# Kernel tuning notes

Measured on AMD Instinct MI355X. Metric: run time of the kernel, lower is better.

Reference implementation:

```python
import jax, jax.numpy as jnp
import numpy as np

N_NODES = 200_000
N_EDGES = 6_400_000


def _gat_head(h, src, dst, W, a, n_nodes):
    """One GAT head: z = h @ W; e = leaky_relu([z_src||z_dst] @ a);
    segment softmax of e over incoming edges of each dst node;
    weighted scatter-add of z_src into dst. W: [Din, Dout], a: [2*Dout]."""
    d = W.shape[1]
    z = h @ W                      # [N, Dout]
    z_src = z[src]                 # [E, Dout] gather
    z_dst = z[dst]                 # [E, Dout] gather
    # [z_src||z_dst] @ a == z_src @ a[:d] + z_dst @ a[d:]  (avoids materializing the cat)
    e = jax.nn.leaky_relu(z_src @ a[:d] + z_dst @ a[d:])  # [E]
    # numerically stable segment softmax grouped by dst
    m = jax.ops.segment_max(e, dst, num_segments=n_nodes)
    m = jnp.where(jnp.isfinite(m), m, 0.0)
    ex = jnp.exp(e - m[dst])
    denom = jax.ops.segment_sum(ex, dst, num_segments=n_nodes)
    alpha = ex / denom[dst]        # [E]
    # weighted scatter-aggregation; isolated dst nodes get zeros (DGL update_all)
    return jax.ops.segment_sum(alpha[:, None] * z_src, dst, num_segments=n_nodes)


def reference(h, src, dst, fc1, attn1, fc2, attn2, mlp_w, mlp_b):
    n = h.shape[0]
    # layer1: 2 heads, hidden_dim=16, merge='cat' -> [N, 32]
    heads = [_gat_head(h, src, dst, fc1[i], attn1[i], n) for i in range(fc1.shape[0])]
    x = jnp.concatenate(heads, axis=1)
    x = jax.nn.elu(x)
    # layer2: 1 head, out_dim=2, cat of single head -> [N, 2]
    x = _gat_head(x, src, dst, fc2, attn2, n)
    # flatten to [1, 2*N], linear, sigmoid
    x = x.reshape(1, -1)
    out = jax.nn.sigmoid(x @ mlp_w + mlp_b)
    return out


def setup_inputs() -> dict:
    key = jax.random.key(0)
    ks = jax.random.split(key, 9)
    h = jax.random.normal(ks[0], (N_NODES, 2), dtype=jnp.float32)
    src = jax.random.randint(ks[1], (N_EDGES,), 0, N_NODES)
    dst = jax.random.randint(ks[2], (N_EDGES,), 0, N_NODES)
    # layer1: 2 heads, fc [in=2 -> out=16] stored as [head, in, out]; attn [head, 2*16]
    fc1 = jax.random.normal(ks[3], (2, 2, 16), dtype=jnp.float32)
    attn1 = jax.random.normal(ks[4], (2, 32), dtype=jnp.float32)
    # layer2: 1 head, fc [32 -> 2]; attn [2*2]
    fc2 = jax.random.normal(ks[5], (32, 2), dtype=jnp.float32)
    attn2 = jax.random.normal(ks[6], (4,), dtype=jnp.float32)
    # final MLP: Linear(2*num_nodes, 1); small scale to keep sigmoid unsaturated
    mlp_w = jax.random.normal(ks[7], (2 * N_NODES, 1), dtype=jnp.float32) * 1e-3
    mlp_b = jax.random.normal(ks[8], (1,), dtype=jnp.float32)
    return {"h": h, "src": src, "dst": dst, "fc1": fc1, "attn1": attn1,
            "fc2": fc2, "attn2": attn2, "mlp_w": mlp_w, "mlp_b": mlp_b}
```

## Files before the change

### kernel.cpp

```cpp
#include <hip/hip_runtime.h>
#include <hip/hip_bf16.h>
#include <math.h>

#define NN 200000
#define NE 6400000

#define BSHIFT 9
#define BNODES 512
#define NB 391
#define CAP 17408
#define NBLK_SC 256
#define SCT 1024
#define CHUNK (NE / NBLK_SC)

#define W_DACC 0
#define W_UV   4
#define W_CUR  16
#define W_NOFF 2048
#define W_NCNT (W_NOFF + NN)
#define W_META (W_NCNT + NN)
#define W_ACC  (W_META + NB*CAP)
#define W_Z2   (W_ACC + 6*NN)
#define W_TOTAL (W_Z2 + 2*NN)

__global__ void k_init(unsigned* __restrict__ ws) {
    int t = blockIdx.x * blockDim.x + threadIdx.x;
    if (t == 0) *(double*)ws = 0.0;
    if (t < NB) ws[W_CUR + t] = 0u;
}

__global__ void k_prep(const float* __restrict__ fc1, const float* __restrict__ attn1,
                       float* __restrict__ uv) {
    int t = threadIdx.x;
    if (t < 8) {
        int h = t >> 2, r = t & 3, i = r & 1, isv = r >> 1;
        double s = 0.0;
        for (int o = 0; o < 16; ++o)
            s += (double)fc1[h * 32 + i * 16 + o] * (double)attn1[h * 32 + isv * 16 + o];
        uv[t] = (float)s;
    }
}

__launch_bounds__(SCT)
__global__ void k_scatter(const int* __restrict__ src, const int* __restrict__ dst,
                          unsigned* __restrict__ meta, unsigned* __restrict__ cur) {
    __shared__ unsigned cnt[NB], gbase[NB];
    for (int i = threadIdx.x; i < NB; i += SCT) cnt[i] = 0u;
    __syncthreads();
    int beg = blockIdx.x * CHUNK;
    unsigned pack[25];
#pragma unroll
    for (int k = 0; k < 25; ++k) {
        int j = k * SCT + threadIdx.x;
        pack[k] = 0xFFFFFFFFu;
        if (j < CHUNK) {
            unsigned d = (unsigned)__builtin_nontemporal_load(dst + beg + j);
            unsigned rank = atomicAdd(&cnt[d >> BSHIFT], 1u);
            pack[k] = d | (rank << 18);
        }
    }
    __syncthreads();
    for (int i = threadIdx.x; i < NB; i += SCT)
        gbase[i] = cnt[i] ? atomicAdd(&cur[i], cnt[i]) : 0u;
    __syncthreads();
#pragma unroll
    for (int k = 0; k < 25; ++k) {
        if (pack[k] != 0xFFFFFFFFu) {
            int j = k * SCT + threadIdx.x;
            unsigned d = pack[k] & 0x3FFFFu;
            unsigned b = d >> BSHIFT;
            unsigned slot = gbase[b] + (pack[k] >> 18);
            if (slot < CAP) {
                unsigned sn = (unsigned)__builtin_nontemporal_load(src + beg + j);
                meta[(size_t)b * CAP + slot] = sn | ((d & (BNODES - 1)) << 18);
            }
        }
    }
}

__launch_bounds__(1024)
__global__ void k_sort(unsigned* __restrict__ meta, const unsigned* __restrict__ cur,
                       unsigned* __restrict__ nodeoff, unsigned* __restrict__ nodecnt) {
    __shared__ unsigned hist[BNODES], base[BNODES], scan[BNODES];
    int b = blockIdx.x, t = threadIdx.x;
    size_t boff = (size_t)b * CAP;
    int cnt = min((int)cur[b], CAP);
    for (int i = t; i < BNODES; i += 1024) hist[i] = 0u;
    __syncthreads();
    unsigned rm[17], rr[17];
#pragma unroll
    for (int k = 0; k < 17; ++k) {
        int i = k * 1024 + t;
        rm[k] = 0xFFFFFFFFu;
        rr[k] = 0u;
        if (i < cnt) {
            rm[k] = meta[boff + i];
            rr[k] = atomicAdd(&hist[rm[k] >> 18], 1u);
        }
    }
    asm volatile("s_waitcnt vmcnt(0)" ::: "memory");
    __syncthreads();
    if (t < BNODES) scan[t] = hist[t];
    __syncthreads();
    for (int d = 1; d < BNODES; d <<= 1) {
        unsigned v = 0u;
        if (t < BNODES && t >= d) v = scan[t - d];
        __syncthreads();
        if (t < BNODES) scan[t] += v;
        __syncthreads();
    }
    int nb = b * BNODES;
    int nn = min(BNODES, NN - nb);
    if (t < BNODES) {
        unsigned ex = scan[t] - hist[t];
        base[t] = ex;
        if (t < nn) {
            nodeoff[nb + t] = (unsigned)boff + ex;
            nodecnt[nb + t] = hist[t];
        }
    }
    __syncthreads();
#pragma unroll
    for (int k = 0; k < 17; ++k)
        if (rm[k] != 0xFFFFFFFFu)
            meta[boff + base[rm[k] >> 18] + rr[k]] = rm[k];
}

__global__ void k_gat1(const unsigned* __restrict__ meta, const unsigned* __restrict__ nodeoff,
                       const unsigned* __restrict__ nodecnt, const float2* __restrict__ h,
                       const float* __restrict__ uv, float* __restrict__ accc) {
    int n = blockIdx.x * blockDim.x + threadIdx.x;
    if (n >= NN) return;
    float u00 = uv[0], u10 = uv[1], v00 = uv[2], v10 = uv[3];
    float u01 = uv[4], u11 = uv[5], v01 = uv[6], v11 = uv[7];
    float2 hd = h[n];
    float c0 = fmaf(hd.x, v00, hd.y * v10);
    float c1 = fmaf(hd.x, v01, hd.y * v11);
    unsigned off = nodeoff[n];
    int cnt = (int)nodecnt[n];
    float s0 = 0.f, s1 = 0.f, s2 = 0.f, s3 = 0.f, s4 = 0.f, s5 = 0.f;
#pragma unroll 4
    for (int k = 0; k < cnt; ++k) {
        unsigned m = meta[(size_t)off + k];
        float2 hs = h[m & 0x3FFFF];
        float e0 = fmaf(hs.x, u00, fmaf(hs.y, u10, c0));
        float e1 = fmaf(hs.x, u01, fmaf(hs.y, u11, c1));
        e0 = e0 >= 0.f ? e0 : 0.01f * e0;
        e1 = e1 >= 0.f ? e1 : 0.01f * e1;
        float ex0 = __expf(e0);
        float ex1 = __expf(e1);
        s0 += ex0; s1 += ex0 * hs.x; s2 += ex0 * hs.y;
        s3 += ex1; s4 += ex1 * hs.x; s5 += ex1 * hs.y;
    }
    accc[(size_t)0 * NN + n] = s0;
    accc[(size_t)1 * NN + n] = s1;
    accc[(size_t)2 * NN + n] = s2;
    accc[(size_t)3 * NN + n] = s3;
    accc[(size_t)4 * NN + n] = s4;
    accc[(size_t)5 * NN + n] = s5;
}

__global__ void k_node1(const float* __restrict__ accc, const float* __restrict__ fc1,
                        const float* __restrict__ fc2, float2* __restrict__ z2) {
    int n = blockIdx.x * blockDim.x + threadIdx.x;
    if (n >= NN) return;
    float a[6];
#pragma unroll
    for (int j = 0; j < 6; ++j) a[j] = accc[(size_t)j * NN + n];
    float den0 = a[0], A0 = a[1], B0 = a[2];
    float den1 = a[3], A1 = a[4], B1 = a[5];
    float x[32];
#pragma unroll
    for (int o = 0; o < 16; ++o) {
        float t0 = den0 > 0.f ? (A0 * fc1[o]      + B0 * fc1[16 + o]) / den0 : 0.f;
        float t1 = den1 > 0.f ? (A1 * fc1[32 + o] + B1 * fc1[48 + o]) / den1 : 0.f;
        x[o]      = t0 > 0.f ? t0 : expm1f(t0);
        x[16 + o] = t1 > 0.f ? t1 : expm1f(t1);
    }
    float z0 = 0.f, z1 = 0.f;
#pragma unroll
    for (int j = 0; j < 32; ++j) {
        z0 += x[j] * fc2[2 * j];
        z1 += x[j] * fc2[2 * j + 1];
    }
    z2[n] = make_float2(z0, z1);
}

__global__ void k_gat2(const unsigned* __restrict__ meta, const unsigned* __restrict__ nodeoff,
                       const unsigned* __restrict__ nodecnt, const float2* __restrict__ z2,
                       const float* __restrict__ attn2, float* __restrict__ acc2c) {
    int n = blockIdx.x * blockDim.x + threadIdx.x;
    if (n >= NN) return;
    float a0 = attn2[0], a1 = attn2[1], a2 = attn2[2], a3 = attn2[3];
    float2 zd = z2[n];
    float cd = fmaf(zd.x, a2, zd.y * a3);
    unsigned off = nodeoff[n];
    int cnt = (int)nodecnt[n];
    float s0 = 0.f, s1 = 0.f, s2 = 0.f;
#pragma unroll 4
    for (int k = 0; k < cnt; ++k) {
        unsigned m = meta[(size_t)off + k];
        float2 zs = z2[m & 0x3FFFF];
        float e = fmaf(zs.x, a0, fmaf(zs.y, a1, cd));
        e = e >= 0.f ? e : 0.01f * e;
        float ex = __expf(e - 48.f);
        s0 += ex; s1 += ex * zs.x; s2 += ex * zs.y;
    }
    acc2c[(size_t)0 * NN + n] = s0;
    acc2c[(size_t)1 * NN + n] = s1;
    acc2c[(size_t)2 * NN + n] = s2;
}

__global__ void k_final(const float* __restrict__ acc2c, const float* __restrict__ mlp_w,
                        double* __restrict__ dacc) {
    int n = blockIdx.x * blockDim.x + threadIdx.x;
    double v = 0.0;
    if (n < NN) {
        float den = acc2c[(size_t)0 * NN + n];
        float n0  = acc2c[(size_t)1 * NN + n];
        float n1  = acc2c[(size_t)2 * NN + n];
        float x0 = den > 0.f ? n0 / den : 0.f;
        float x1 = den > 0.f ? n1 / den : 0.f;
        v = (double)x0 * (double)mlp_w[2 * n] + (double)x1 * (double)mlp_w[2 * n + 1];
    }
    for (int off = 32; off > 0; off >>= 1) v += __shfl_down(v, off);
    __shared__ double sm[4];
    int lane = threadIdx.x & 63, wid = threadIdx.x >> 6;
    if (lane == 0) sm[wid] = v;
    __syncthreads();
    if (threadIdx.x == 0) {
        double sum = sm[0] + sm[1] + sm[2] + sm[3];
        unsafeAtomicAdd(dacc, sum);
    }
}

__global__ void k_out(const double* __restrict__ dacc, const float* __restrict__ mlp_b,
                      float* __restrict__ out) {
    double logit = dacc[0] + (double)mlp_b[0];
    out[0] = (float)(1.0 / (1.0 + exp(-logit)));
}

extern "C" void kernel_launch(void* const* d_in, const int* in_sizes, int n_in,
                              void* d_out, int out_size, void* d_ws, size_t ws_size,
                              hipStream_t stream) {
    const float* h     = (const float*)d_in[0];
    const int*   src   = (const int*)d_in[1];
    const int*   dst   = (const int*)d_in[2];
    const float* fc1   = (const float*)d_in[3];
    const float* attn1 = (const float*)d_in[4];
    const float* fc2   = (const float*)d_in[5];
    const float* attn2 = (const float*)d_in[6];
    const float* mlp_w = (const float*)d_in[7];
    const float* mlp_b = (const float*)d_in[8];
    float* out = (float*)d_out;

    unsigned* ws      = (unsigned*)d_ws;
    double*   dacc    = (double*)d_ws;
    float*    uv      = (float*)(ws + W_UV);
    unsigned* cur     = ws + W_CUR;
    unsigned* nodeoff = ws + W_NOFF;
    unsigned* nodecnt = ws + W_NCNT;
    unsigned* meta    = ws + W_META;
    float*    accc    = (float*)(ws + W_ACC);
    float2*   z2      = (float2*)(ws + W_Z2);

    const int NG = (NN + 255) / 256;

    hipLaunchKernelGGL(k_init, dim3(2), dim3(256), 0, stream, ws);
    hipLaunchKernelGGL(k_prep, dim3(1), dim3(64), 0, stream, fc1, attn1, uv);
    hipLaunchKernelGGL(k_scatter, dim3(NBLK_SC), dim3(SCT), 0, stream,
                       src, dst, meta, cur);
    hipLaunchKernelGGL(k_sort, dim3(NB), dim3(1024), 0, stream,
                       meta, cur, nodeoff, nodecnt);
    hipLaunchKernelGGL(k_gat1, dim3(NG), dim3(256), 0, stream,
                       meta, nodeoff, nodecnt, (const float2*)h, uv, accc);
    hipLaunchKernelGGL(k_node1, dim3(NG), dim3(256), 0, stream, accc, fc1, fc2, z2);
    hipLaunchKernelGGL(k_gat2, dim3(NG), dim3(256), 0, stream,
                       meta, nodeoff, nodecnt, (const float2*)z2, attn2, accc);
    hipLaunchKernelGGL(k_final, dim3(NG), dim3(256), 0, stream, accc, mlp_w, dacc);
    hipLaunchKernelGGL(k_out, dim3(1), dim3(1), 0, stream, dacc, mlp_b, out);
}
```

Before: 250.6 us.

## Fuse node update into GAT passes and resize destination buckets to match CUs

The per-node layer-1 epilogue (normalise, ELU, project through fc2) moves into k_gat1. The layer-2 normalise and MLP reduction moves into k_gat2. This drops two launches and the intermediate accumulator arrays written to and reread from global memory. The destination bucketing changes from 391 buckets of 512 nodes to 256 buckets of 782 nodes, so k_sort runs one block per CU with more registers per thread. Non-power-of-two buckets need an integer divide in the scatter, and larger per-block sorts raise register pressure.

```diff
diff --git a/kernel.cpp b/kernel.cpp
--- a/kernel.cpp
+++ b/kernel.cpp
@@ -5,22 +5,21 @@
 #define NN 200000
 #define NE 6400000
 
-#define BSHIFT 9
-#define BNODES 512
-#define NB 391
-#define CAP 17408
+#define BNODES 782
+#define NB 256
+#define CAP 27648
 #define NBLK_SC 256
 #define SCT 1024
 #define CHUNK (NE / NBLK_SC)
+#define SREG 27
 
 #define W_DACC 0
 #define W_UV   4
 #define W_CUR  16
-#define W_NOFF 2048
+#define W_NOFF 1024
 #define W_NCNT (W_NOFF + NN)
 #define W_META (W_NCNT + NN)
-#define W_ACC  (W_META + NB*CAP)
-#define W_Z2   (W_ACC + 6*NN)
+#define W_Z2   (W_META + NB*CAP)
 #define W_TOTAL (W_Z2 + 2*NN)
 
 __global__ void k_init(unsigned* __restrict__ ws) {
@@ -55,7 +54,7 @@
         pack[k] = 0xFFFFFFFFu;
         if (j < CHUNK) {
             unsigned d = (unsigned)__builtin_nontemporal_load(dst + beg + j);
-            unsigned rank = atomicAdd(&cnt[d >> BSHIFT], 1u);
+            unsigned rank = atomicAdd(&cnt[d / BNODES], 1u);
             pack[k] = d | (rank << 18);
         }
     }
@@ -68,29 +67,30 @@
         if (pack[k] != 0xFFFFFFFFu) {
             int j = k * SCT + threadIdx.x;
             unsigned d = pack[k] & 0x3FFFFu;
-            unsigned b = d >> BSHIFT;
+            unsigned b = d / BNODES;
+            unsigned dl = d - b * BNODES;
             unsigned slot = gbase[b] + (pack[k] >> 18);
             if (slot < CAP) {
                 unsigned sn = (unsigned)__builtin_nontemporal_load(src + beg + j);
-                meta[(size_t)b * CAP + slot] = sn | ((d & (BNODES - 1)) << 18);
+                meta[(size_t)b * CAP + slot] = sn | (dl << 18);
             }
         }
     }
 }
 
-__launch_bounds__(1024)
+__launch_bounds__(SCT)
 __global__ void k_sort(unsigned* __restrict__ meta, const unsigned* __restrict__ cur,
                        unsigned* __restrict__ nodeoff, unsigned* __restrict__ nodecnt) {
     __shared__ unsigned hist[BNODES], base[BNODES], scan[BNODES];
     int b = blockIdx.x, t = threadIdx.x;
     size_t boff = (size_t)b * CAP;
     int cnt = min((int)cur[b], CAP);
-    for (int i = t; i < BNODES; i += 1024) hist[i] = 0u;
-    __syncthreads();
-    unsigned rm[17], rr[17];
-#pragma unroll
-    for (int k = 0; k < 17; ++k) {
-        int i = k * 1024 + t;
+    for (int i = t; i < BNODES; i += SCT) hist[i] = 0u;
+    __syncthreads();
+    unsigned rm[SREG], rr[SREG];
+#pragma unroll
+    for (int k = 0; k < SREG; ++k) {
+        int i = k * SCT + t;
         rm[k] = 0xFFFFFFFFu;
         rr[k] = 0u;
         if (i < cnt) {
@@ -121,14 +121,15 @@
     }
     __syncthreads();
 #pragma unroll
-    for (int k = 0; k < 17; ++k)
+    for (int k = 0; k < SREG; ++k)
         if (rm[k] != 0xFFFFFFFFu)
             meta[boff + base[rm[k] >> 18] + rr[k]] = rm[k];
 }
 
 __global__ void k_gat1(const unsigned* __restrict__ meta, const unsigned* __restrict__ nodeoff,
                        const unsigned* __restrict__ nodecnt, const float2* __restrict__ h,
-                       const float* __restrict__ uv, float* __restrict__ accc) {
+                       const float* __restrict__ uv, const float* __restrict__ fc1,
+                       const float* __restrict__ fc2, float2* __restrict__ z2) {
     int n = blockIdx.x * blockDim.x + threadIdx.x;
     if (n >= NN) return;
     float u00 = uv[0], u10 = uv[1], v00 = uv[2], v10 = uv[3];
@@ -152,75 +153,43 @@
         s0 += ex0; s1 += ex0 * hs.x; s2 += ex0 * hs.y;
         s3 += ex1; s4 += ex1 * hs.x; s5 += ex1 * hs.y;
     }
-    accc[(size_t)0 * NN + n] = s0;
-    accc[(size_t)1 * NN + n] = s1;
-    accc[(size_t)2 * NN + n] = s2;
-    accc[(size_t)3 * NN + n] = s3;
-    accc[(size_t)4 * NN + n] = s4;
-    accc[(size_t)5 * NN + n] = s5;
-}
-
-__global__ void k_node1(const float* __restrict__ accc, const float* __restrict__ fc1,
-                        const float* __restrict__ fc2, float2* __restrict__ z2) {
-    int n = blockIdx.x * blockDim.x + threadIdx.x;
-    if (n >= NN) return;
-    float a[6];
-#pragma unroll
-    for (int j = 0; j < 6; ++j) a[j] = accc[(size_t)j * NN + n];
-    float den0 = a[0], A0 = a[1], B0 = a[2];
-    float den1 = a[3], A1 = a[4], B1 = a[5];
-    float x[32];
+    float z0 = 0.f, z1 = 0.f;
 #pragma unroll
     for (int o = 0; o < 16; ++o) {
-        float t0 = den0 > 0.f ? (A0 * fc1[o]      + B0 * fc1[16 + o]) / den0 : 0.f;
-        float t1 = den1 > 0.f ? (A1 * fc1[32 + o] + B1 * fc1[48 + o]) / den1 : 0.f;
-        x[o]      = t0 > 0.f ? t0 : expm1f(t0);
-        x[16 + o] = t1 > 0.f ? t1 : expm1f(t1);
-    }
-    float z0 = 0.f, z1 = 0.f;
-#pragma unroll
-    for (int j = 0; j < 32; ++j) {
-        z0 += x[j] * fc2[2 * j];
-        z1 += x[j] * fc2[2 * j + 1];
+        float t0 = s0 > 0.f ? (s1 * fc1[o]      + s2 * fc1[16 + o]) / s0 : 0.f;
+        float t1 = s3 > 0.f ? (s4 * fc1[32 + o] + s5 * fc1[48 + o]) / s3 : 0.f;
+        float x0 = t0 > 0.f ? t0 : expm1f(t0);
+        float x1 = t1 > 0.f ? t1 : expm1f(t1);
+        z0 += x0 * fc2[2 * o]      + x1 * fc2[2 * (16 + o)];
+        z1 += x0 * fc2[2 * o + 1]  + x1 * fc2[2 * (16 + o) + 1];
     }
     z2[n] = make_float2(z0, z1);
 }
 
 __global__ void k_gat2(const unsigned* __restrict__ meta, const unsigned* __restrict__ nodeoff,
                        const unsigned* __restrict__ nodecnt, const float2* __restrict__ z2,
-                       const float* __restrict__ attn2, float* __restrict__ acc2c) {
-    int n = blockIdx.x * blockDim.x + threadIdx.x;
-    if (n >= NN) return;
-    float a0 = attn2[0], a1 = attn2[1], a2 = attn2[2], a3 = attn2[3];
-    float2 zd = z2[n];
-    float cd = fmaf(zd.x, a2, zd.y * a3);
-    unsigned off = nodeoff[n];
-    int cnt = (int)nodecnt[n];
-    float s0 = 0.f, s1 = 0.f, s2 = 0.f;
-#pragma unroll 4
-    for (int k = 0; k < cnt; ++k) {
-        unsigned m = meta[(size_t)off + k];
-        float2 zs = z2[m & 0x3FFFF];
-        float e = fmaf(zs.x, a0, fmaf(zs.y, a1, cd));
-        e = e >= 0.f ? e : 0.01f * e;
-        float ex = __expf(e - 48.f);
-        s0 += ex; s1 += ex * zs.x; s2 += ex * zs.y;
-    }
-    acc2c[(size_t)0 * NN + n] = s0;
-    acc2c[(size_t)1 * NN + n] = s1;
-    acc2c[(size_t)2 * NN + n] = s2;
-}
-
-__global__ void k_final(const float* __restrict__ acc2c, const float* __restrict__ mlp_w,
-                        double* __restrict__ dacc) {
+                       const float* __restrict__ attn2, const float* __restrict__ mlp_w,
+                       double* __restrict__ dacc) {
     int n = blockIdx.x * blockDim.x + threadIdx.x;
     double v = 0.0;
     if (n < NN) {
-        float den = acc2c[(size_t)0 * NN + n];
-        float n0  = acc2c[(size_t)1 * NN + n];
-        float n1  = acc2c[(size_t)2 * NN + n];
-        float x0 = den > 0.f ? n0 / den : 0.f;
-        float x1 = den > 0.f ? n1 / den : 0.f;
+        float a0 = attn2[0], a1 = attn2[1], a2 = attn2[2], a3 = attn2[3];
+        float2 zd = z2[n];
+        float cd = fmaf(zd.x, a2, zd.y * a3);
+        unsigned off = nodeoff[n];
+        int cnt = (int)nodecnt[n];
+        float s0 = 0.f, s1 = 0.f, s2 = 0.f;
+#pragma unroll 4
+        for (int k = 0; k < cnt; ++k) {
+            unsigned m = meta[(size_t)off + k];
+            float2 zs = z2[m & 0x3FFFF];
+            float e = fmaf(zs.x, a0, fmaf(zs.y, a1, cd));
+            e = e >= 0.f ? e : 0.01f * e;
+            float ex = __expf(e - 48.f);
+            s0 += ex; s1 += ex * zs.x; s2 += ex * zs.y;
+        }
+        float x0 = s0 > 0.f ? s1 / s0 : 0.f;
+        float x1 = s0 > 0.f ? s2 / s0 : 0.f;
         v = (double)x0 * (double)mlp_w[2 * n] + (double)x1 * (double)mlp_w[2 * n + 1];
     }
     for (int off = 32; off > 0; off >>= 1) v += __shfl_down(v, off);
@@ -261,22 +230,19 @@
     unsigned* nodeoff = ws + W_NOFF;
     unsigned* nodecnt = ws + W_NCNT;
     unsigned* meta    = ws + W_META;
-    float*    accc    = (float*)(ws + W_ACC);
     float2*   z2      = (float2*)(ws + W_Z2);
 
     const int NG = (NN + 255) / 256;
 
-    hipLaunchKernelGGL(k_init, dim3(2), dim3(256), 0, stream, ws);
+    hipLaunchKernelGGL(k_init, dim3(1), dim3(256), 0, stream, ws);
     hipLaunchKernelGGL(k_prep, dim3(1), dim3(64), 0, stream, fc1, attn1, uv);
     hipLaunchKernelGGL(k_scatter, dim3(NBLK_SC), dim3(SCT), 0, stream,
                        src, dst, meta, cur);
-    hipLaunchKernelGGL(k_sort, dim3(NB), dim3(1024), 0, stream,
+    hipLaunchKernelGGL(k_sort, dim3(NB), dim3(SCT), 0, stream,
                        meta, cur, nodeoff, nodecnt);
     hipLaunchKernelGGL(k_gat1, dim3(NG), dim3(256), 0, stream,
-                       meta, nodeoff, nodecnt, (const float2*)h, uv, accc);
-    hipLaunchKernelGGL(k_node1, dim3(NG), dim3(256), 0, stream, accc, fc1, fc2, z2);
+                       meta, nodeoff, nodecnt, (const float2*)h, uv, fc1, fc2, z2);
     hipLaunchKernelGGL(k_gat2, dim3(NG), dim3(256), 0, stream,
-                       meta, nodeoff, nodecnt, (const float2*)z2, attn2, accc);
-    hipLaunchKernelGGL(k_final, dim3(NG), dim3(256), 0, stream, accc, mlp_w, dacc);
+                       meta, nodeoff, nodecnt, (const float2*)z2, attn2, mlp_w, dacc);
     hipLaunchKernelGGL(k_out, dim3(1), dim3(1), 0, stream, dacc, mlp_b, out);
 }
```

Result: faster. 240.7 us (-3.9%).
